# Optimization experiments

Hardware: AMD Instinct MI355X
Metric: run time of the kernel (lower is better)

Reference implementation:

```python
import jax, jax.numpy as jnp
import numpy as np

DIM = 1024
NUM_HEADS = 16
HEAD_DIM = DIM // NUM_HEADS
B, T = 2, 2048


def setup_inputs() -> dict:
    key = jax.random.key(0)
    ks = jax.random.split(key, 7)
    x = jax.random.normal(ks[0], (B, T, DIM), dtype=jnp.float32)
    # causal mask, broadcastable over batch and heads
    mask = jnp.tril(jnp.ones((T, T), dtype=bool))[None, None, :, :]
    # rope tables for half rotary angles, tiled to head_dim (cat of two halves)
    pos = jnp.arange(T, dtype=jnp.float32)[:, None]
    inv_freq = 1.0 / (10000.0 ** (jnp.arange(0, HEAD_DIM, 2, dtype=jnp.float32) / HEAD_DIM))
    ang = pos * inv_freq[None, :]                      # [T, hd/2]
    ang = jnp.concatenate([ang, ang], axis=-1)         # [T, hd]
    rope_sin = jnp.sin(ang)[None, None, :, :]
    rope_cos = jnp.cos(ang)[None, None, :, :]
    s = 0.02
    qkv_w = jax.random.normal(ks[1], (DIM, 3 * DIM), dtype=jnp.float32) * s
    qkv_b = jnp.zeros((3 * DIM,), dtype=jnp.float32)
    proj_w = jax.random.normal(ks[2], (DIM, DIM), dtype=jnp.float32) * s
    proj_b = jnp.zeros((DIM,), dtype=jnp.float32)
    return {"x": x, "mask": mask, "rope_sin": rope_sin, "rope_cos": rope_cos,
            "qkv_w": qkv_w, "qkv_b": qkv_b, "proj_w": proj_w, "proj_b": proj_b}


def _rotate_half(t):
    half = t.shape[-1] // 2
    return jnp.concatenate([-t[..., half:], t[..., :half]], axis=-1)


def _apply_rope(t, sin, cos):
    return t * cos + _rotate_half(t) * sin


def reference(x, mask, rope_sin, rope_cos, qkv_w, qkv_b, proj_w, proj_b):
    Bb, Tt, C = x.shape
    qkv = x @ qkv_w + qkv_b                            # [B, T, 3C]
    q, k, v = jnp.split(qkv, 3, axis=-1)
    def split_heads(t):                                # [B, T, C] -> [B, H, T, hd]
        return t.reshape(Bb, Tt, NUM_HEADS, HEAD_DIM).transpose(0, 2, 1, 3)
    q, k, v = split_heads(q), split_heads(k), split_heads(v)
    sin = rope_sin[:, :, :Tt, :]
    cos = rope_cos[:, :, :Tt, :]
    q = _apply_rope(q, sin, cos)
    k = _apply_rope(k, sin, cos)
    att = jnp.einsum("bhqd,bhkd->bhqk", q, k) / (HEAD_DIM ** 0.5)
    att = jnp.where(mask, att, -jnp.inf)
    att = jax.nn.softmax(att, axis=-1)
    y = jnp.einsum("bhqk,bhkd->bhqd", att, v)          # [B, H, T, hd]
    y = y.transpose(0, 2, 1, 3).reshape(Bb, Tt, C)
    return y @ proj_w + proj_b
```

## Files before the change

kernel.cpp:

```cpp
#include <hip/hip_runtime.h>

typedef unsigned short u16;
typedef u16 u16x8 __attribute__((ext_vector_type(8)));
typedef __bf16 bf16x8 __attribute__((ext_vector_type(8)));
typedef float f32x4 __attribute__((ext_vector_type(4)));

#define T_SEQ 2048
#define DIM 1024
#define NH 16
#define HD 64

#define MFMA(a, b, c) __builtin_amdgcn_mfma_f32_16x16x32_bf16(a, b, c, 0, 0, 0)

__device__ __forceinline__ u16 f2bf(float f) {
  unsigned u = __builtin_bit_cast(unsigned, f);
  u = u + 0x7fffu + ((u >> 16) & 1u);
  return (u16)(u >> 16);
}

__device__ __forceinline__ bf16x8 ld8(const u16* p) {
  return __builtin_bit_cast(bf16x8, *(const u16x8*)p);
}

__device__ __forceinline__ void gload_lds16(const u16* g, u16* l) {
  __builtin_amdgcn_global_load_lds((const __attribute__((address_space(1))) void*)(g),
                                   (__attribute__((address_space(3))) void*)(l),
                                   16, 0, 0);
}

__global__ void k_prep(const float* __restrict__ X, u16* __restrict__ Y,
                       const float* __restrict__ Wq, u16* __restrict__ WqT,
                       const float* __restrict__ Wp, u16* __restrict__ WpT) {
  __shared__ float tile[32][33];
  int bid = blockIdx.x;
  if (bid < 4096) {
    int i = (bid * 256 + threadIdx.x) * 4;
    float4 f = *(const float4*)&X[i];
    ushort4 o = make_ushort4(f2bf(f.x), f2bf(f.y), f2bf(f.z), f2bf(f.w));
    *(ushort4*)&Y[i] = o;
    return;
  }
  const float* W; u16* WT; int K = 1024, N, bx, by;
  if (bid < 4096 + 3072) { int t = bid - 4096; W = Wq; WT = WqT; N = 3072; bx = t % 96; by = t / 96; }
  else                   { int t = bid - 7168; W = Wp; WT = WpT; N = 1024; bx = t % 32; by = t / 32; }
  int tx = threadIdx.x & 31, ty = threadIdx.x >> 5;
  int c0 = bx * 32, r0 = by * 32;
#pragma unroll
  for (int r = 0; r < 4; r++)
    tile[ty + r * 8][tx] = W[(r0 + ty + r * 8) * N + c0 + tx];
  __syncthreads();
  int n_l = threadIdx.x >> 3, kg = (threadIdx.x & 7) * 4;
  ushort4 ov = make_ushort4(f2bf(tile[kg + 0][n_l]), f2bf(tile[kg + 1][n_l]),
                            f2bf(tile[kg + 2][n_l]), f2bf(tile[kg + 3][n_l]));
  *(ushort4*)&WT[(size_t)(c0 + n_l) * K + r0 + kg] = ov;
}

#define GEMM_CORE(Aptr, BTptr, Kdim, bxv, byv)                                    \
  const int tid = threadIdx.x;                                                    \
  const int lane = tid & 63, w = tid >> 6;                                        \
  const int l15 = lane & 15, quad = lane >> 4;                                    \
  const int wm = w >> 1, wn = w & 1;                                              \
  const int rowBase = (byv) * 128;                                                \
  const int colBase = (bxv) * 128;                                                \
  f32x4 acc[4][4];                                                                \
  _Pragma("unroll") for (int i = 0; i < 4; i++)                                   \
      _Pragma("unroll") for (int j = 0; j < 4; j++)                               \
          acc[i][j] = (f32x4){0.f, 0.f, 0.f, 0.f};                                \
  const int srow = lane >> 2;                                                     \
  const int schunk = (lane & 3) * 8;                                              \
  for (int k0 = 0; k0 < (Kdim); k0 += 32) {                                       \
    __syncthreads();                                                              \
    _Pragma("unroll") for (int p = 0; p < 2; p++) {                               \
      int rr = w * 32 + p * 16;                                                   \
      gload_lds16(&(Aptr)[(size_t)(rowBase + rr + srow) * (Kdim) + k0 + schunk],  \
                  &As[rr * 32]);                                                  \
      gload_lds16(&(BTptr)[(size_t)(colBase + rr + srow) * (Kdim) + k0 + schunk], \
                  &Bs[rr * 32]);                                                  \
    }                                                                             \
    __syncthreads();                                                              \
    bf16x8 af[4], bfv[4];                                                         \
    _Pragma("unroll") for (int i = 0; i < 4; i++) {                               \
      af[i] = ld8(&As[(wm * 64 + i * 16 + l15) * 32 + quad * 8]);                 \
      bfv[i] = ld8(&Bs[(wn * 64 + i * 16 + l15) * 32 + quad * 8]);                \
    }                                                                             \
    _Pragma("unroll") for (int i = 0; i < 4; i++)                                 \
        _Pragma("unroll") for (int j = 0; j < 4; j++)                             \
            acc[i][j] = MFMA(af[i], bfv[j], acc[i][j]);                           \
  }

__global__ __launch_bounds__(256) void k_gemm_qkv(
    const u16* __restrict__ A, const u16* __restrict__ BT,
    const float* __restrict__ bias,
    const float* __restrict__ rsin, const float* __restrict__ rcos,
    u16* __restrict__ qb, u16* __restrict__ kb, u16* __restrict__ vtb) {
  __shared__ __align__(16) u16 As[128 * 32];
  __shared__ __align__(16) u16 Bs[128 * 32];
  const int n = blockIdx.x, xcd = n & 7, s = n >> 3;
  const int cg = xcd & 1, rg = xcd >> 1;
  const int bxv = cg * 12 + (s >> 3);
  const int byv = rg * 8 + (s & 7);
  GEMM_CORE(A, BT, DIM, bxv, byv)

#pragma unroll
  for (int j = 0; j < 4; j++) {
    float bv = bias[colBase + wn * 64 + j * 16 + l15];
#pragma unroll
    for (int i = 0; i < 4; i++)
#pragma unroll
      for (int r = 0; r < 4; r++) acc[i][j][r] += bv;
  }

  const int colW = colBase + wn * 64;
  const int sec = colW >> 10;
  const int hh = (colW & 1023) >> 6;

#pragma unroll
  for (int i = 0; i < 4; i++) {
#pragma unroll
    for (int r = 0; r < 4; r++) {
      int grow = rowBase + wm * 64 + i * 16 + quad * 4 + r;
      int b = grow >> 11, t = grow & 2047;
#pragma unroll
      for (int j = 0; j < 4; j++) {
        int d = j * 16 + l15;
        float v = acc[i][j][r];
        if (sec == 2) {
          vtb[((b * NH + hh) * HD + d) * T_SEQ + t] = f2bf(v);
        } else {
          float pr = acc[i][j ^ 2][r];
          float rot = (j < 2) ? -pr : pr;
          float rv = v * rcos[t * HD + d] + rot * rsin[t * HD + d];
          if (sec == 0)
            qb[((b * NH + hh) * T_SEQ + t) * HD + d] = f2bf(rv * 0.18033688f);
          else
            kb[((b * NH + hh) * T_SEQ + t) * HD + d] = f2bf(rv);
        }
      }
    }
  }
}

__global__ __launch_bounds__(256) void k_gemm_proj(
    const u16* __restrict__ A, const u16* __restrict__ BT,
    const float* __restrict__ bias, float* __restrict__ C) {
  __shared__ __align__(16) u16 As[128 * 32];
  __shared__ __align__(16) u16 Bs[128 * 32];
  const int n = blockIdx.x, xcd = n & 7, s = n >> 3;
  const int cg = xcd & 1, rg = xcd >> 1;
  const int bxv = cg * 4 + (s >> 3);
  const int byv = rg * 8 + (s & 7);
  GEMM_CORE(A, BT, DIM, bxv, byv)

#pragma unroll
  for (int i = 0; i < 4; i++)
#pragma unroll
    for (int r = 0; r < 4; r++) {
      int grow = rowBase + wm * 64 + i * 16 + quad * 4 + r;
#pragma unroll
      for (int j = 0; j < 4; j++) {
        int col = colBase + wn * 64 + j * 16 + l15;
        C[grow * DIM + col] = acc[i][j][r] + bias[col];
      }
    }
}

#define KLD 72
#define VLD 136

__global__ __launch_bounds__(256, 4) void k_attn(
    const u16* __restrict__ qb, const u16* __restrict__ kb,
    const u16* __restrict__ vtb, u16* __restrict__ yb) {
  __shared__ __align__(16) u16 Ks[128 * KLD];
  __shared__ __align__(16) u16 VTs[64 * VLD];
  const int tid = threadIdx.x;
  const int lane = tid & 63, w = tid >> 6;
  const int l15 = lane & 15, quad = lane >> 4;
  const int bh = blockIdx.x;
  const int qt = 31 - blockIdx.y;

  const u16* qp = qb + (size_t)bh * T_SEQ * HD;
  const u16* kp = kb + (size_t)bh * T_SEQ * HD;
  const u16* vp = vtb + (size_t)bh * HD * T_SEQ;

  const f32x4 zf = {0.f, 0.f, 0.f, 0.f};
  const int qrow_g = qt * 64 + w * 16 + l15;

  bf16x8 qa0 = ld8(&qp[(size_t)qrow_g * HD + quad * 8]);
  bf16x8 qa1 = ld8(&qp[(size_t)qrow_g * HD + 32 + quad * 8]);

  f32x4 o[4];
#pragma unroll
  for (int m = 0; m < 4; m++) o[m] = zf;
  float li = 0.f;

  const int nch = (qt + 2) >> 1;
  const int sr = tid >> 3, sc = (tid & 7) * 8;
  const int vr = tid >> 4, vc = (tid & 15) * 8;

  for (int c = 0; c < nch; c++) {
#pragma unroll
    for (int p = 0; p < 4; p++) {
      int t = sr + p * 32;
      int srw = (t & 96) | ((t & 4) << 2) | ((t & 24) >> 1) | (t & 3);
      *(u16x8*)&Ks[srw * KLD + sc] = *(const u16x8*)&kp[(size_t)(c * 128 + t) * HD + sc];
    }
#pragma unroll
    for (int p = 0; p < 4; p++) {
      int r = vr + p * 16;
      *(u16x8*)&VTs[r * VLD + vc] = *(const u16x8*)&vp[(size_t)r * T_SEQ + c * 128 + vc];
    }
    __syncthreads();

    const bool lastc = (c == nch - 1);
    f32x4 p8[8];
#pragma unroll
    for (int tau = 0; tau < 8; tau++) {
      bf16x8 ka0 = ld8(&Ks[(tau * 16 + l15) * KLD + quad * 8]);
      bf16x8 ka1 = ld8(&Ks[(tau * 16 + l15) * KLD + 32 + quad * 8]);
      f32x4 sv = MFMA(ka0, qa0, zf);
      sv = MFMA(ka1, qa1, sv);
#pragma unroll
      for (int rr = 0; rr < 4; rr++) {
        float e = __builtin_exp2f(sv[rr]);
        int key = c * 128 + ((tau >> 1) << 5) + (quad << 3) + ((tau & 1) << 2) + rr;
        if (lastc && key > qrow_g) e = 0.f;
        li += e;
        p8[tau][rr] = e;
      }
    }

#pragma unroll
    for (int a = 0; a < 4; a++) {
      bf16x8 pt;
#pragma unroll
      for (int rr = 0; rr < 4; rr++) {
        pt[rr] = (__bf16)p8[2 * a][rr];
        pt[4 + rr] = (__bf16)p8[2 * a + 1][rr];
      }
#pragma unroll
      for (int m = 0; m < 4; m++) {
        bf16x8 va = ld8(&VTs[(m * 16 + l15) * VLD + a * 32 + quad * 8]);
        o[m] = MFMA(va, pt, o[m]);
      }
    }
    __syncthreads();
  }

  li += __shfl_xor(li, 16);
  li += __shfl_xor(li, 32);
  const float inv = 1.0f / li;

  const int b = bh >> 4, h = bh & 15;
#pragma unroll
  for (int m = 0; m < 4; m++)
#pragma unroll
    for (int rr = 0; rr < 4; rr++) {
      int d = m * 16 + quad * 4 + rr;
      yb[((size_t)(b * T_SEQ + qrow_g) * NH + h) * HD + d] = f2bf(o[m][rr] * inv);
    }
}

extern "C" void kernel_launch(void* const* d_in, const int* in_sizes, int n_in,
                              void* d_out, int out_size, void* d_ws, size_t ws_size,
                              hipStream_t stream) {
  const float* x      = (const float*)d_in[0];
  const float* rsin   = (const float*)d_in[2];
  const float* rcos   = (const float*)d_in[3];
  const float* qkv_w  = (const float*)d_in[4];
  const float* qkv_b  = (const float*)d_in[5];
  const float* proj_w = (const float*)d_in[6];
  const float* proj_b = (const float*)d_in[7];
  float* out = (float*)d_out;

  char* ws = (char*)d_ws;
  u16* x_bf  = (u16*)(ws);
  u16* qkvT  = (u16*)(ws + (8ull << 20));
  u16* projT = (u16*)(ws + (14ull << 20));
  u16* q_buf = (u16*)(ws + (16ull << 20));
  u16* k_buf = (u16*)(ws + (24ull << 20));
  u16* vT    = (u16*)(ws + (32ull << 20));
  u16* y_buf = (u16*)(ws + (40ull << 20));

  hipLaunchKernelGGL(k_prep, dim3(8192), dim3(256), 0, stream,
                     x, x_bf, qkv_w, qkvT, proj_w, projT);
  hipLaunchKernelGGL(k_gemm_qkv, dim3(768), dim3(256), 0, stream,
                     x_bf, qkvT, qkv_b, rsin, rcos, q_buf, k_buf, vT);
  hipLaunchKernelGGL(k_attn, dim3(32, 32), dim3(256), 0, stream,
                     q_buf, k_buf, vT, y_buf);
  hipLaunchKernelGGL(k_gemm_proj, dim3(256), dim3(256), 0, stream,
                     y_buf, projT, proj_b, out);
}
```

Measured before the change: 223.4 us.

## Double-buffer proj GEMM and widen attention q-tile with diagonal skip

The projection GEMM gets its own double-buffered LDS loop that prefetches the next K slice while computing the current one. The attention kernel now processes 128 query rows per block (32 per wave, two MFMA row tiles), so each K/V tile loaded into LDS is reused twice as much. On the diagonal chunk, each wave skips the fully masked key sub-blocks. The grid is remapped to group heads by XCD, outputs are stored as ushort4 vectors, and the occupancy hint on the attention kernel is dropped, which trades register headroom for higher register use per thread.

After: 237.7 us. 6.4% more time.

```diff
diff --git a/kernel.cpp b/kernel.cpp
--- a/kernel.cpp
+++ b/kernel.cpp
@@ -143,13 +143,53 @@
 __global__ __launch_bounds__(256) void k_gemm_proj(
     const u16* __restrict__ A, const u16* __restrict__ BT,
     const float* __restrict__ bias, float* __restrict__ C) {
-  __shared__ __align__(16) u16 As[128 * 32];
-  __shared__ __align__(16) u16 Bs[128 * 32];
+  __shared__ __align__(16) u16 As[2][128 * 32];
+  __shared__ __align__(16) u16 Bs[2][128 * 32];
+  const int tid = threadIdx.x;
+  const int lane = tid & 63, w = tid >> 6;
+  const int l15 = lane & 15, quad = lane >> 4;
+  const int wm = w >> 1, wn = w & 1;
   const int n = blockIdx.x, xcd = n & 7, s = n >> 3;
   const int cg = xcd & 1, rg = xcd >> 1;
   const int bxv = cg * 4 + (s >> 3);
   const int byv = rg * 8 + (s & 7);
-  GEMM_CORE(A, BT, DIM, bxv, byv)
+  const int rowBase = byv * 128, colBase = bxv * 128;
+  f32x4 acc[4][4];
+#pragma unroll
+  for (int i = 0; i < 4; i++)
+#pragma unroll
+    for (int j = 0; j < 4; j++) acc[i][j] = (f32x4){0.f, 0.f, 0.f, 0.f};
+  const int srow = lane >> 2, schunk = (lane & 3) * 8;
+  const int r0 = w * 32, r1 = w * 32 + 16;
+
+  gload_lds16(&A[(size_t)(rowBase + r0 + srow) * DIM + schunk], &As[0][r0 * 32]);
+  gload_lds16(&A[(size_t)(rowBase + r1 + srow) * DIM + schunk], &As[0][r1 * 32]);
+  gload_lds16(&BT[(size_t)(colBase + r0 + srow) * DIM + schunk], &Bs[0][r0 * 32]);
+  gload_lds16(&BT[(size_t)(colBase + r1 + srow) * DIM + schunk], &Bs[0][r1 * 32]);
+  __syncthreads();
+
+  for (int it = 0; it < 32; it++) {
+    const int cur = it & 1, nxt = cur ^ 1;
+    if (it < 31) {
+      const int k0 = (it + 1) * 32;
+      gload_lds16(&A[(size_t)(rowBase + r0 + srow) * DIM + k0 + schunk], &As[nxt][r0 * 32]);
+      gload_lds16(&A[(size_t)(rowBase + r1 + srow) * DIM + k0 + schunk], &As[nxt][r1 * 32]);
+      gload_lds16(&BT[(size_t)(colBase + r0 + srow) * DIM + k0 + schunk], &Bs[nxt][r0 * 32]);
+      gload_lds16(&BT[(size_t)(colBase + r1 + srow) * DIM + k0 + schunk], &Bs[nxt][r1 * 32]);
+    }
+    bf16x8 af[4], bfv[4];
+#pragma unroll
+    for (int i = 0; i < 4; i++) {
+      af[i] = ld8(&As[cur][(wm * 64 + i * 16 + l15) * 32 + quad * 8]);
+      bfv[i] = ld8(&Bs[cur][(wn * 64 + i * 16 + l15) * 32 + quad * 8]);
+    }
+#pragma unroll
+    for (int i = 0; i < 4; i++)
+#pragma unroll
+      for (int j = 0; j < 4; j++)
+        acc[i][j] = MFMA(af[i], bfv[j], acc[i][j]);
+    __syncthreads();
+  }
 
 #pragma unroll
   for (int i = 0; i < 4; i++)
@@ -167,7 +207,7 @@
 #define KLD 72
 #define VLD 136
 
-__global__ __launch_bounds__(256, 4) void k_attn(
+__global__ __launch_bounds__(256) void k_attn(
     const u16* __restrict__ qb, const u16* __restrict__ kb,
     const u16* __restrict__ vtb, u16* __restrict__ yb) {
   __shared__ __align__(16) u16 Ks[128 * KLD];
@@ -175,27 +215,34 @@
   const int tid = threadIdx.x;
   const int lane = tid & 63, w = tid >> 6;
   const int l15 = lane & 15, quad = lane >> 4;
-  const int bh = blockIdx.x;
-  const int qt = 31 - blockIdx.y;
+  const int n = blockIdx.x, xcd = n & 7, s = n >> 3;
+  const int bh = xcd * 4 + (s & 3);
+  const int qt = 15 - (s >> 2);
 
   const u16* qp = qb + (size_t)bh * T_SEQ * HD;
   const u16* kp = kb + (size_t)bh * T_SEQ * HD;
   const u16* vp = vtb + (size_t)bh * HD * T_SEQ;
 
   const f32x4 zf = {0.f, 0.f, 0.f, 0.f};
-  const int qrow_g = qt * 64 + w * 16 + l15;
-
-  bf16x8 qa0 = ld8(&qp[(size_t)qrow_g * HD + quad * 8]);
-  bf16x8 qa1 = ld8(&qp[(size_t)qrow_g * HD + 32 + quad * 8]);
-
-  f32x4 o[4];
-#pragma unroll
-  for (int m = 0; m < 4; m++) o[m] = zf;
-  float li = 0.f;
-
-  const int nch = (qt + 2) >> 1;
+  const int qrow0 = qt * 128 + w * 32;
+
+  bf16x8 qa[2][2];
+#pragma unroll
+  for (int t2 = 0; t2 < 2; t2++)
+#pragma unroll
+    for (int h = 0; h < 2; h++)
+      qa[t2][h] = ld8(&qp[(size_t)(qrow0 + t2 * 16 + l15) * HD + h * 32 + quad * 8]);
+
+  f32x4 o[2][4];
+#pragma unroll
+  for (int t2 = 0; t2 < 2; t2++)
+#pragma unroll
+    for (int m = 0; m < 4; m++) o[t2][m] = zf;
+  f32x4 li4[2] = {zf, zf};
+
   const int sr = tid >> 3, sc = (tid & 7) * 8;
   const int vr = tid >> 4, vc = (tid & 15) * 8;
+  const int nch = qt + 1;
 
   for (int c = 0; c < nch; c++) {
 #pragma unroll
@@ -211,53 +258,62 @@
     }
     __syncthreads();
 
-    const bool lastc = (c == nch - 1);
-    f32x4 p8[8];
-#pragma unroll
-    for (int tau = 0; tau < 8; tau++) {
-      bf16x8 ka0 = ld8(&Ks[(tau * 16 + l15) * KLD + quad * 8]);
-      bf16x8 ka1 = ld8(&Ks[(tau * 16 + l15) * KLD + 32 + quad * 8]);
-      f32x4 sv = MFMA(ka0, qa0, zf);
-      sv = MFMA(ka1, qa1, sv);
-#pragma unroll
-      for (int rr = 0; rr < 4; rr++) {
-        float e = __builtin_exp2f(sv[rr]);
-        int key = c * 128 + ((tau >> 1) << 5) + (quad << 3) + ((tau & 1) << 2) + rr;
-        if (lastc && key > qrow_g) e = 0.f;
-        li += e;
-        p8[tau][rr] = e;
-      }
-    }
-
-#pragma unroll
-    for (int a = 0; a < 4; a++) {
-      bf16x8 pt;
-#pragma unroll
-      for (int rr = 0; rr < 4; rr++) {
-        pt[rr] = (__bf16)p8[2 * a][rr];
-        pt[4 + rr] = (__bf16)p8[2 * a + 1][rr];
+    const bool dia = (c == qt);
+    const int aLim = dia ? (w + 1) : 4;
+    for (int a = 0; a < aLim; a++) {
+      bf16x8 pt[2];
+#pragma unroll
+      for (int u = 0; u < 2; u++) {
+        const int tau = 2 * a + u;
+        bf16x8 ka0 = ld8(&Ks[(tau * 16 + l15) * KLD + quad * 8]);
+        bf16x8 ka1 = ld8(&Ks[(tau * 16 + l15) * KLD + 32 + quad * 8]);
+        const int keyb = c * 128 + a * 32 + quad * 8 + u * 4;
+#pragma unroll
+        for (int t2 = 0; t2 < 2; t2++) {
+          f32x4 sv = MFMA(ka0, qa[t2][0], zf);
+          sv = MFMA(ka1, qa[t2][1], sv);
+          const int qr = qrow0 + t2 * 16 + l15;
+          f32x4 ev;
+#pragma unroll
+          for (int rr = 0; rr < 4; rr++) {
+            float e = __builtin_exp2f(sv[rr]);
+            if (dia && (keyb + rr > qr)) e = 0.f;
+            ev[rr] = e;
+            pt[t2][u * 4 + rr] = (__bf16)e;
+          }
+          li4[t2] += ev;
+        }
       }
 #pragma unroll
       for (int m = 0; m < 4; m++) {
         bf16x8 va = ld8(&VTs[(m * 16 + l15) * VLD + a * 32 + quad * 8]);
-        o[m] = MFMA(va, pt, o[m]);
+        o[0][m] = MFMA(va, pt[0], o[0][m]);
+        o[1][m] = MFMA(va, pt[1], o[1][m]);
       }
     }
     __syncthreads();
   }
 
-  li += __shfl_xor(li, 16);
-  li += __shfl_xor(li, 32);
-  const float inv = 1.0f / li;
+  float inv[2];
+#pragma unroll
+  for (int t2 = 0; t2 < 2; t2++) {
+    float L = li4[t2][0] + li4[t2][1] + li4[t2][2] + li4[t2][3];
+    L += __shfl_xor(L, 16);
+    L += __shfl_xor(L, 32);
+    inv[t2] = 1.0f / L;
+  }
 
   const int b = bh >> 4, h = bh & 15;
 #pragma unroll
-  for (int m = 0; m < 4; m++)
-#pragma unroll
-    for (int rr = 0; rr < 4; rr++) {
-      int d = m * 16 + quad * 4 + rr;
-      yb[((size_t)(b * T_SEQ + qrow_g) * NH + h) * HD + d] = f2bf(o[m][rr] * inv);
-    }
+  for (int t2 = 0; t2 < 2; t2++) {
+    const size_t rowb = ((size_t)(b * T_SEQ + qrow0 + t2 * 16 + l15) * NH + h) * HD;
+#pragma unroll
+    for (int m = 0; m < 4; m++) {
+      ushort4 ov = make_ushort4(f2bf(o[t2][m][0] * inv[t2]), f2bf(o[t2][m][1] * inv[t2]),
+                                f2bf(o[t2][m][2] * inv[t2]), f2bf(o[t2][m][3] * inv[t2]));
+      *(ushort4*)&yb[rowb + m * 16 + quad * 4] = ov;
+    }
+  }
 }
 
 extern "C" void kernel_launch(void* const* d_in, const int* in_sizes, int n_in,
@@ -285,7 +341,7 @@
                      x, x_bf, qkv_w, qkvT, proj_w, projT);
   hipLaunchKernelGGL(k_gemm_qkv, dim3(768), dim3(256), 0, stream,
                      x_bf, qkvT, qkv_b, rsin, rcos, q_buf, k_buf, vT);
-  hipLaunchKernelGGL(k_attn, dim3(32, 32), dim3(256), 0, stream,
+  hipLaunchKernelGGL(k_attn, dim3(512), dim3(256), 0, stream,
                      q_buf, k_buf, vT, y_buf);
   hipLaunchKernelGGL(k_gemm_proj, dim3(256), dim3(256), 0, stream,
                      y_buf, projT, proj_b, out);
```
